# Performance work log

Hardware: AMD Instinct MI355X
Metric: run time of the kernel (lower is better)

Reference implementation:

```python
import jax, jax.numpy as jnp
import numpy as np

D_MODEL, NHEAD, D_K = 512, 8, 64
MIN_RBF, MAX_RBF = 0.1, 0.9
MIN_SPREAD, MAX_SPREAD, BASE = 1.0, 6.0, 20.0
LN_EPS = 1e-5


def _layernorm(x, w, b):
    mu = jnp.mean(x, axis=-1, keepdims=True)
    var = jnp.var(x, axis=-1, keepdims=True)
    return (x - mu) * jax.lax.rsqrt(var + LN_EPS) * w + b


def setup_inputs() -> dict:
    key = jax.random.key(0)
    ks = jax.random.split(key, 10)
    B, N = 1, 2048
    inp = {
        "q": jax.random.normal(ks[0], (B, N, D_MODEL), jnp.float32),
        "k": jax.random.normal(ks[1], (B, N, D_MODEL), jnp.float32),
        "v": jax.random.normal(ks[2], (B, N, D_MODEL), jnp.float32),
        "coords": jax.random.normal(ks[3], (B, N, 3), jnp.float32) * 3.0,
        "key_padding_mask": jnp.zeros((B, N), bool),
        # learned params (torch.randn init for projections, LN defaults)
        "q_proj": jax.random.normal(ks[4], (NHEAD, D_MODEL, D_K), jnp.float32),
        "k_proj": jax.random.normal(ks[5], (NHEAD, D_MODEL, D_K), jnp.float32),
        "v_proj": jax.random.normal(ks[6], (NHEAD, D_MODEL, D_K), jnp.float32),
        "q_ln_w": jnp.ones((D_K,), jnp.float32), "q_ln_b": jnp.zeros((D_K,), jnp.float32),
        "k_ln_w": jnp.ones((D_K,), jnp.float32), "k_ln_b": jnp.zeros((D_K,), jnp.float32),
        "v_ln_w": jnp.ones((D_K,), jnp.float32), "v_ln_b": jnp.zeros((D_K,), jnp.float32),
        "out_w": jax.random.normal(ks[7], (D_MODEL, D_MODEL), jnp.float32) / np.sqrt(D_MODEL),
        "out_b": jnp.zeros((D_MODEL,), jnp.float32),
    }
    return inp


def reference(q, k, v, coords, key_padding_mask,
              q_proj, k_proj, v_proj,
              q_ln_w, q_ln_b, k_ln_w, k_ln_b, v_ln_w, v_ln_b,
              out_w, out_b):
    B, N, _ = q.shape
    # per-head projections: [B,H,N,dk]
    Q = _layernorm(jnp.einsum('bnd,hdk->bhnk', q, q_proj), q_ln_w, q_ln_b)
    K = _layernorm(jnp.einsum('bnd,hdk->bhnk', k, k_proj), k_ln_w, k_ln_b)
    V = _layernorm(jnp.einsum('bnd,hdk->bhnk', v, v_proj), v_ln_w, v_ln_b)

    # head-specific gaussian spreads (torch.logspace(0,1,H,base) semantics)
    spreads = MIN_SPREAD + (MAX_SPREAD - MIN_SPREAD) * (BASE ** jnp.linspace(0.0, 1.0, NHEAD) - 1.0) / (BASE - 1.0)

    # pairwise squared distances [B,N,N] -> per-head RBF [B,H,N,N]
    d2 = jnp.sum((coords[:, :, None, :] - coords[:, None, :, :]) ** 2, axis=-1)
    rbf = jnp.exp(-d2[:, None, :, :] / (2.0 * spreads[None, :, None, None] ** 2))
    rbf = jnp.clip(rbf, MIN_RBF, MAX_RBF)

    # RBF-modulated scaled dot-product attention
    scores = jnp.einsum('bhik,bhjk->bhij', Q, K) / np.sqrt(D_K) * rbf
    scores = jnp.where(key_padding_mask[:, None, None, :], -1e9, scores)
    P = jax.nn.softmax(scores, axis=-1)
    out = jnp.einsum('bhij,bhjk->bhik', P, V)  # [B,H,N,dk]

    # torch: out.permute(0,2,3,1).reshape(B,N,d_model)
    out = jnp.transpose(out, (0, 2, 3, 1)).reshape(B, N, D_MODEL)
    return out @ out_w.T + out_b
```

## Files before the change

### kernel.cpp

```cpp
#include <hip/hip_runtime.h>
#include <math.h>

#define N_TOK 2048
#define D_MODEL 512
#define NHEAD 8
#define DK 64
#define LOG2E 1.44269504f
#define QSCALE 0.18033688f
#define KTILE 6144
#define KHEAD (32 * KTILE)

typedef __attribute__((ext_vector_type(8))) short short8;
typedef __attribute__((ext_vector_type(4))) short short4v;
typedef __attribute__((ext_vector_type(4))) float f32x4;
typedef __attribute__((ext_vector_type(16))) float f32x16;
typedef __attribute__((ext_vector_type(4))) unsigned int u32x4;

__device__ __forceinline__ short f2bf(float x) {
    unsigned u = __float_as_uint(x);
    u = (u + 0x7fffu + ((u >> 16) & 1u)) >> 16;
    return (short)u;
}

__device__ __forceinline__ float bf2f(short s) {
    return __uint_as_float(((unsigned)(unsigned short)s) << 16);
}

__device__ __forceinline__ void split2(float x, short& h_, short& l_) {
    h_ = f2bf(x);
    l_ = f2bf(x - bf2f(h_));
}

__device__ __forceinline__ void split3(float x, short& h_, short& m_, short& l_) {
    h_ = f2bf(x);
    float r = x - bf2f(h_);
    m_ = f2bf(r);
    l_ = f2bf(r - bf2f(m_));
}

__device__ __forceinline__ unsigned cvt_pk_bf16(float lo, float hi) {
    unsigned r;
    asm("v_cvt_pk_bf16_f32 %0, %1, %2" : "=v"(r) : "v"(lo), "v"(hi));
    return r;
}

__device__ __forceinline__ float head_c(int h) {
    float tt = (float)h * (1.0f / 7.0f);
    float sp = 1.0f + 5.0f * (__builtin_exp2f(tt * 4.3219281f) - 1.0f) * (1.0f / 19.0f);
    return -LOG2E / (2.0f * sp * sp);
}

__global__ __launch_bounds__(256) void prep_all_kernel(
    const float* __restrict__ coords, const unsigned char* __restrict__ mask,
    const float* __restrict__ qp, const float* __restrict__ kp,
    const float* __restrict__ vp, const float* __restrict__ ow,
    short* __restrict__ Wt, short* __restrict__ Wo,
    short* __restrict__ Kf, float* __restrict__ mpen,
    unsigned* __restrict__ tflag)
{
    __shared__ float tile[64][65];
    const int bid = blockIdx.x;
    const int t = threadIdx.x;

    if (bid < 256) {
        int i = bid;
        int z = i >> 6;
        int bx = i & 7, by = (i >> 3) & 7;
        if (z == 3) {
            int m0 = bx * 64, j0 = by * 64, hh = by;
            for (int ii = t; ii < 4096; ii += 256) {
                int r = ii >> 6, kk = ii & 63;
                Wo[(size_t)(m0 + r) * 512 + j0 + kk] =
                    f2bf(ow[(size_t)(m0 + r) * 512 + kk * 8 + hh]);
            }
            return;
        }
        const float* src = z == 0 ? qp : (z == 1 ? kp : vp);
        const int h = bx, d0 = by * 64;
        for (int ii = t; ii < 4096; ii += 256) {
            int r = ii >> 6, c = ii & 63;
            tile[r][c] = src[((size_t)h * 512 + d0 + r) * 64 + c];
        }
        __syncthreads();
        short* W = Wt + (size_t)z * 512 * 512;
        for (int ii = t; ii < 4096; ii += 256) {
            int cr = ii >> 6, dc_ = ii & 63;
            W[(size_t)(h * 64 + cr) * 512 + d0 + dc_] = f2bf(tile[dc_][cr]);
        }
    } else {
        int j = (bid - 256) * 256 + t;
        float x = coords[j * 3 + 0], y = coords[j * 3 + 1], z = coords[j * 3 + 2];
        unsigned char mk = mask[j];
        mpen[j] = mk ? -1e9f : 0.f;
        unsigned long long b = __ballot(mk != 0);
        if ((t & 63) == 0) tflag[j >> 6] = (b != 0ull) ? 1u : 0u;
        float n2 = x * x + y * y + z * z;
        const short one = (short)0x3F80;
        const int s = (j & 63) >> 5;
        const int m = j & 31;
        #pragma unroll
        for (int h = 0; h < NHEAD; ++h) {
            float c = head_c(h);
            short ahx, alx, ahy, aly, ahz, alz, k2a, k2b, k2c;
            split2(-2.f * c * x, ahx, alx);
            split2(-2.f * c * y, ahy, aly);
            split2(-2.f * c * z, ahz, alz);
            split3(c * n2, k2a, k2b, k2c);
            short8 g0, g1, g2, g3;
            g0[0] = ahx; g0[1] = alx; g0[2] = ahx; g0[3] = ahy;
            g0[4] = aly; g0[5] = ahy; g0[6] = ahz; g0[7] = alz;
            g1[0] = ahz; g1[1] = alx; g1[2] = aly; g1[3] = alz;
            g1[4] = k2a; g1[5] = k2b; g1[6] = k2c; g1[7] = one;
            g2[0] = one; g2[1] = one;
            #pragma unroll
            for (int e = 2; e < 8; ++e) g2[e] = 0;
            #pragma unroll
            for (int e = 0; e < 8; ++e) g3[e] = 0;
            short* base = Kf + (size_t)h * KHEAD + (size_t)(j >> 6) * KTILE
                        + 4096 + (size_t)s * 1024;
            *(short8*)(base + (size_t)m * 8) = g0;
            *(short8*)(base + (size_t)(m + 32) * 8) = g1;
            *(short8*)(base + 512 + (size_t)m * 8) = g2;
            *(short8*)(base + 512 + (size_t)(m + 32) * 8) = g3;
        }
    }
}

__global__ __launch_bounds__(256) void proj_ln_mfma_kernel(
    const float* __restrict__ xq, const float* __restrict__ xk,
    const float* __restrict__ xv, const short* __restrict__ Wt,
    const float* __restrict__ qlw, const float* __restrict__ qlb,
    const float* __restrict__ klw, const float* __restrict__ klb,
    const float* __restrict__ vlw, const float* __restrict__ vlb,
    short* __restrict__ Qf, short* __restrict__ Kf, short* __restrict__ Vf)
{
    __shared__ short Xs[128 * 64];
    __shared__ short Ws[64 * 64];
    const int z = blockIdx.z, h = blockIdx.y;
    const int n0 = blockIdx.x * 128;
    const int tid = threadIdx.x, w = tid >> 6, l = tid & 63;
    const int l15 = l & 15, lg = l >> 4;

    const float* X = z == 0 ? xq : (z == 1 ? xk : xv);
    const short* Wz = Wt + ((size_t)z * 512 + h * 64) * 512;

    const f32x4 zero4 = {0.f, 0.f, 0.f, 0.f};
    f32x4 acc[2][4];
    #pragma unroll
    for (int H = 0; H < 2; ++H)
        #pragma unroll
        for (int dc = 0; dc < 4; ++dc) acc[H][dc] = zero4;

    for (int kb = 0; kb < 8; ++kb) {
        const int d0 = kb * 64;
        __syncthreads();
        #pragma unroll
        for (int i = 0; i < 8; ++i) {
            int idx = tid + i * 256;
            int r = idx >> 4;
            int f = idx & 15;
            float4 xv4 = *(const float4*)(X + (size_t)(n0 + r) * 512 + d0 + f * 4);
            short4v pk;
            pk[0] = f2bf(xv4.x); pk[1] = f2bf(xv4.y);
            pk[2] = f2bf(xv4.z); pk[3] = f2bf(xv4.w);
            *(short4v*)(Xs + r * 64 + (((f >> 1) * 8) ^ ((r & 7) << 3)) + (f & 1) * 4) = pk;
        }
        #pragma unroll
        for (int i = 0; i < 2; ++i) {
            int c = tid + i * 256;
            int r = c >> 3, g = c & 7;
            short8 wv = *(const short8*)(Wz + (size_t)r * 512 + d0 + g * 8);
            *(short8*)(Ws + r * 64 + ((g * 8) ^ ((r & 7) << 3))) = wv;
        }
        __syncthreads();
        const int arowA = w * 16 + l15;
        const int arowB = 64 + arowA;
        const int asw = (arowA & 7) << 3;
        short8 aA0 = *(const short8*)(Xs + arowA * 64 + ((lg * 8) ^ asw));
        short8 aA1 = *(const short8*)(Xs + arowA * 64 + ((32 + lg * 8) ^ asw));
        short8 aB0 = *(const short8*)(Xs + arowB * 64 + ((lg * 8) ^ asw));
        short8 aB1 = *(const short8*)(Xs + arowB * 64 + ((32 + lg * 8) ^ asw));
        #pragma unroll
        for (int dc = 0; dc < 4; ++dc) {
            const int brow = dc * 16 + l15;
            short8 b0 = *(const short8*)(Ws + brow * 64 + ((lg * 8) ^ ((brow & 7) << 3)));
            short8 b1 = *(const short8*)(Ws + brow * 64 + ((32 + lg * 8) ^ ((brow & 7) << 3)));
            acc[0][dc] = __builtin_amdgcn_mfma_f32_16x16x32_bf16(aA0, b0, acc[0][dc], 0, 0, 0);
            acc[0][dc] = __builtin_amdgcn_mfma_f32_16x16x32_bf16(aA1, b1, acc[0][dc], 0, 0, 0);
            acc[1][dc] = __builtin_amdgcn_mfma_f32_16x16x32_bf16(aB0, b0, acc[1][dc], 0, 0, 0);
            acc[1][dc] = __builtin_amdgcn_mfma_f32_16x16x32_bf16(aB1, b1, acc[1][dc], 0, 0, 0);
        }
    }

    const float* lw  = z == 0 ? qlw : (z == 1 ? klw : vlw);
    const float* lbp = z == 0 ? qlb : (z == 1 ? klb : vlb);
    float wv_[4], bv_[4];
    #pragma unroll
    for (int dc = 0; dc < 4; ++dc) {
        wv_[dc] = lw[dc * 16 + l15];
        bv_[dc] = lbp[dc * 16 + l15];
    }

    #pragma unroll
    for (int H = 0; H < 2; ++H) {
        const int nb = n0 + H * 64;
        const int kt = nb >> 6;
        float mu[4], rs[4];
        #pragma unroll
        for (int reg = 0; reg < 4; ++reg) {
            float s = acc[H][0][reg] + acc[H][1][reg] + acc[H][2][reg] + acc[H][3][reg];
            #pragma unroll
            for (int off = 1; off < 16; off <<= 1) s += __shfl_xor(s, off);
            float m = s * (1.0f / 64.0f);
            float ss = 0.f;
            #pragma unroll
            for (int dc = 0; dc < 4; ++dc) { float d = acc[H][dc][reg] - m; ss += d * d; }
            #pragma unroll
            for (int off = 1; off < 16; off <<= 1) ss += __shfl_xor(ss, off);
            mu[reg] = m;
            rs[reg] = rsqrtf(ss * (1.0f / 64.0f) + 1e-5f);
        }
        if (z == 0) {
            short* Qh = Qf + (size_t)h * (N_TOK * DK);
            #pragma unroll
            for (int dc = 0; dc < 4; ++dc)
                #pragma unroll
                for (int reg = 0; reg < 4; ++reg) {
                    int n = nb + w * 16 + lg * 4 + reg;
                    float val = ((acc[H][dc][reg] - mu[reg]) * rs[reg] * wv_[dc] + bv_[dc]) * QSCALE;
                    size_t addr = (size_t)(n >> 5) * 2048 + dc * 512
                                + ((n & 31) + 32 * (l15 >> 3)) * 8 + (l15 & 7);
                    Qh[addr] = f2bf(val);
                }
        } else if (z == 1) {
            short* Kh = Kf + (size_t)h * KHEAD;
            const int sA = w >> 1;
            const int mA = (w & 1) * 16 + lg * 4;
            #pragma unroll
            for (int dc = 0; dc < 4; ++dc)
                #pragma unroll
                for (int reg = 0; reg < 4; ++reg) {
                    float val = (acc[H][dc][reg] - mu[reg]) * rs[reg] * wv_[dc] + bv_[dc];
                    size_t addr = (size_t)kt * KTILE + sA * 2048 + dc * 512
                                + (mA + reg + 32 * (l15 >> 3)) * 8 + (l15 & 7);
                    Kh[addr] = f2bf(val);
                }
        } else {
            short* Vh = Vf + (size_t)h * (N_TOK * DK);
            const int kc = w;
            const int g = lg >> 1;
            const int e0 = (lg & 1) * 4;
            #pragma unroll
            for (int dc = 0; dc < 4; ++dc) {
                int dt = dc >> 1;
                int m = (dc & 1) * 16 + l15;
                short4v p;
                #pragma unroll
                for (int reg = 0; reg < 4; ++reg)
                    p[reg] = f2bf((acc[H][dc][reg] - mu[reg]) * rs[reg] * wv_[dc] + bv_[dc]);
                size_t addr = (size_t)kt * 4096 + dt * 2048 + kc * 512
                            + (m + 32 * g) * 8 + e0;
                *(short4v*)(Vh + addr) = p;
            }
        }
    }
}

__global__ __launch_bounds__(256) void attn_kernel(
    const short* __restrict__ Qf, const short* __restrict__ Kf,
    const short* __restrict__ Vf, const float* __restrict__ coords,
    const float* __restrict__ mpen, const unsigned* __restrict__ tflag,
    short* __restrict__ PO, float* __restrict__ PL)
{
    __shared__ float bufO[2][32][65];
    __shared__ float bufL[2][32];

    const int tid = threadIdx.x;
    const int w = tid >> 6, l = tid & 63;
    const int q31 = l & 31;
    const bool hi = (l >= 32);
    const int rbase = hi ? 4 : 0;
    const int bid = blockIdx.x;
    const int h  = bid & 7;
    const int qt = (bid >> 3) & 63;
    const int z  = bid >> 9;
    const int n0 = qt * 32;

    const short* qbase = Qf + (size_t)h * (N_TOK * DK) + (size_t)qt * 2048 + l * 8;
    short8 qf[4];
    #pragma unroll
    for (int c = 0; c < 4; ++c) qf[c] = *(const short8*)(qbase + c * 512);

    const float ch = head_c(h);
    const int qn = n0 + q31;
    const float qx = coords[qn * 3 + 0];
    const float qy = coords[qn * 3 + 1];
    const float qz = coords[qn * 3 + 2];
    const float cq2 = ch * (qx * qx + qy * qy + qz * qz);
    short8 qaug0, qaug1;
    {
        const short one = (short)0x3F80;
        short qhx, qlx, qhy, qly, qhz, qlz, q2a, q2b, q2c;
        split2(qx, qhx, qlx);
        split2(qy, qhy, qly);
        split2(qz, qhz, qlz);
        split3(cq2, q2a, q2b, q2c);
        if (!hi) {
            qaug0[0] = qhx; qaug0[1] = qhx; qaug0[2] = qlx; qaug0[3] = qhy;
            qaug0[4] = qhy; qaug0[5] = qly; qaug0[6] = qhz; qaug0[7] = qhz;
            qaug1[0] = q2b; qaug1[1] = q2c;
            #pragma unroll
            for (int e = 2; e < 8; ++e) qaug1[e] = 0;
        } else {
            qaug0[0] = qlz; qaug0[1] = qlx; qaug0[2] = qly; qaug0[3] = qlz;
            qaug0[4] = one; qaug0[5] = one; qaug0[6] = one; qaug0[7] = q2a;
            #pragma unroll
            for (int e = 0; e < 8; ++e) qaug1[e] = 0;
        }
    }

    const f32x16 zero16 = {0,0,0,0, 0,0,0,0, 0,0,0,0, 0,0,0,0};
    f32x16 oacc0 = zero16, oacc1 = zero16;
    float l_ = 0.f;

    const short* Kfh = Kf + (size_t)h * KHEAD;
    const short* Vfh = Vf + (size_t)h * (N_TOK * DK);

    for (int t = 0; t < 4; ++t) {
        const int kt = z * 16 + w * 4 + t;
        const int kbase = kt * 64;
        #pragma unroll
        for (int s = 0; s < 2; ++s) {
            const short* kp = Kfh + (size_t)kt * KTILE + s * 2048 + l * 8;
            const short* ap = Kfh + (size_t)kt * KTILE + 4096 + s * 1024 + l * 8;
            const short* vp = Vfh + (size_t)kt * 4096 + s * 1024 + l * 8;

            f32x16 sacc = zero16, aacc = zero16;
            #pragma unroll
            for (int c = 0; c < 4; ++c) {
                short8 kfr = *(const short8*)(kp + c * 512);
                sacc = __builtin_amdgcn_mfma_f32_32x32x16_bf16(kfr, qf[c], sacc, 0, 0, 0);
            }
            {
                short8 a0 = *(const short8*)(ap);
                short8 a1 = *(const short8*)(ap + 512);
                aacc = __builtin_amdgcn_mfma_f32_32x32x16_bf16(a0, qaug0, aacc, 0, 0, 0);
                aacc = __builtin_amdgcn_mfma_f32_32x32x16_bf16(a1, qaug1, aacc, 0, 0, 0);
            }

            #pragma unroll
            for (int r = 0; r < 16; ++r) {
                float rb = __builtin_exp2f(aacc[r]);
                rb = fminf(fmaxf(rb, 0.1f), 0.9f);
                sacc[r] *= rb;
            }
            if (tflag[kt]) {
                #pragma unroll
                for (int r = 0; r < 16; ++r)
                    sacc[r] += mpen[kbase + s * 32 + ((r & 3) + 8 * (r >> 2) + rbase)];
            }

            #pragma unroll
            for (int r = 0; r < 16; ++r) sacc[r] = __builtin_exp2f(sacc[r]);
            {
                float s01 = (sacc[0] + sacc[1]) + (sacc[2] + sacc[3]);
                float s23 = (sacc[4] + sacc[5]) + (sacc[6] + sacc[7]);
                float s45 = (sacc[8] + sacc[9]) + (sacc[10] + sacc[11]);
                float s67 = (sacc[12] + sacc[13]) + (sacc[14] + sacc[15]);
                l_ += (s01 + s23) + (s45 + s67);
            }

            unsigned U0 = cvt_pk_bf16(sacc[0], sacc[1]);
            unsigned U1 = cvt_pk_bf16(sacc[2], sacc[3]);
            unsigned U2 = cvt_pk_bf16(sacc[4], sacc[5]);
            unsigned U3 = cvt_pk_bf16(sacc[6], sacc[7]);
            unsigned U4 = cvt_pk_bf16(sacc[8], sacc[9]);
            unsigned U5 = cvt_pk_bf16(sacc[10], sacc[11]);
            unsigned U6 = cvt_pk_bf16(sacc[12], sacc[13]);
            unsigned U7 = cvt_pk_bf16(sacc[14], sacc[15]);
            unsigned W0 = (unsigned)__shfl_xor((int)U0, 32);
            unsigned W1 = (unsigned)__shfl_xor((int)U1, 32);
            unsigned W2 = (unsigned)__shfl_xor((int)U2, 32);
            unsigned W3 = (unsigned)__shfl_xor((int)U3, 32);
            unsigned W4 = (unsigned)__shfl_xor((int)U4, 32);
            unsigned W5 = (unsigned)__shfl_xor((int)U5, 32);
            unsigned W6 = (unsigned)__shfl_xor((int)U6, 32);
            unsigned W7 = (unsigned)__shfl_xor((int)U7, 32);

            u32x4 b0v, b1v;
            b0v[0] = hi ? W2 : U0;  b0v[1] = hi ? W3 : U1;
            b0v[2] = hi ? U2 : W0;  b0v[3] = hi ? U3 : W1;
            b1v[0] = hi ? W6 : U4;  b1v[1] = hi ? W7 : U5;
            b1v[2] = hi ? U6 : W4;  b1v[3] = hi ? U7 : W5;
            short8 pb0 = __builtin_bit_cast(short8, b0v);
            short8 pb1 = __builtin_bit_cast(short8, b1v);

            {
                short8 v00 = *(const short8*)(vp);
                short8 v01 = *(const short8*)(vp + 512);
                short8 v10 = *(const short8*)(vp + 2048);
                short8 v11 = *(const short8*)(vp + 2048 + 512);
                oacc0 = __builtin_amdgcn_mfma_f32_32x32x16_bf16(v00, pb0, oacc0, 0, 0, 0);
                oacc0 = __builtin_amdgcn_mfma_f32_32x32x16_bf16(v01, pb1, oacc0, 0, 0, 0);
                oacc1 = __builtin_amdgcn_mfma_f32_32x32x16_bf16(v10, pb0, oacc1, 0, 0, 0);
                oacc1 = __builtin_amdgcn_mfma_f32_32x32x16_bf16(v11, pb1, oacc1, 0, 0, 0);
            }
        }
    }

    l_ += __shfl_xor(l_, 32);

    if (w >= 2) {
        int slot = w - 2;
        if (!hi) bufL[slot][q31] = l_;
        #pragma unroll
        for (int r = 0; r < 16; ++r) {
            int d = (r & 3) + 8 * (r >> 2) + rbase;
            bufO[slot][q31][d] = oacc0[r];
            bufO[slot][q31][32 + d] = oacc1[r];
        }
    }
    __syncthreads();
    if (w < 2) {
        l_ += bufL[w][q31];
        #pragma unroll
        for (int r = 0; r < 16; ++r) {
            int d = (r & 3) + 8 * (r >> 2) + rbase;
            oacc0[r] += bufO[w][q31][d];
            oacc1[r] += bufO[w][q31][32 + d];
        }
    }
    __syncthreads();
    if (w == 1) {
        if (!hi) bufL[0][q31] = l_;
        #pragma unroll
        for (int r = 0; r < 16; ++r) {
            int d = (r & 3) + 8 * (r >> 2) + rbase;
            bufO[0][q31][d] = oacc0[r];
            bufO[0][q31][32 + d] = oacc1[r];
        }
    }
    __syncthreads();
    if (w == 0) {
        l_ += bufL[0][q31];
        size_t p = ((size_t)z * NHEAD + h) * N_TOK + n0 + q31;
        if (!hi) PL[p] = l_;
        #pragma unroll
        for (int r = 0; r < 16; ++r) {
            int d = (r & 3) + 8 * (r >> 2) + rbase;
            PO[p * 64 + d] = f2bf(oacc0[r] + bufO[0][q31][d]);
            PO[p * 64 + 32 + d] = f2bf(oacc1[r] + bufO[0][q31][32 + d]);
        }
    }
}

__global__ __launch_bounds__(256) void out_proj_kernel(
    const short* __restrict__ PO, const float* __restrict__ PL,
    const short* __restrict__ Wo, const float* __restrict__ bias,
    float* __restrict__ out)
{
    __shared__ short As[64 * 64];
    __shared__ short Bs[64 * 64];
    const int n0 = blockIdx.x * 64, m0 = blockIdx.y * 64;
    const int tid = threadIdx.x, w = tid >> 6, l = tid & 63;
    const int l15 = l & 15, lg = l >> 4;

    const f32x4 zero4 = {0.f, 0.f, 0.f, 0.f};
    f32x4 acc[4];
    #pragma unroll
    for (int dc = 0; dc < 4; ++dc) acc[dc] = zero4;

    for (int kb = 0; kb < 8; ++kb) {
        const int j0 = kb * 64;
        __syncthreads();
        #pragma unroll
        for (int i = 0; i < 2; ++i) {
            int c = tid + i * 256;
            int r = c >> 3, g = c & 7;
            int n = n0 + r;
            size_t p0 = (size_t)kb * N_TOK + n;
            size_t p1 = (size_t)(NHEAD + kb) * N_TOK + n;
            float rl = 1.0f / (PL[p0] + PL[p1]);
            short8 a0 = *(const short8*)(PO + p0 * 64 + g * 8);
            short8 a1 = *(const short8*)(PO + p1 * 64 + g * 8);
            short8 av;
            #pragma unroll
            for (int e = 0; e < 8; ++e)
                av[e] = f2bf((bf2f(a0[e]) + bf2f(a1[e])) * rl);
            *(short8*)(As + r * 64 + ((g * 8) ^ ((r & 7) << 3))) = av;
            short8 bv = *(const short8*)(Wo + (size_t)(m0 + r) * 512 + j0 + g * 8);
            *(short8*)(Bs + r * 64 + ((g * 8) ^ ((r & 7) << 3))) = bv;
        }
        __syncthreads();
        const int arow = w * 16 + l15;
        short8 a0 = *(const short8*)(As + arow * 64 + ((lg * 8) ^ ((arow & 7) << 3)));
        short8 a1 = *(const short8*)(As + arow * 64 + ((32 + lg * 8) ^ ((arow & 7) << 3)));
        #pragma unroll
        for (int dc = 0; dc < 4; ++dc) {
            const int brow = dc * 16 + l15;
            short8 b0 = *(const short8*)(Bs + brow * 64 + ((lg * 8) ^ ((brow & 7) << 3)));
            acc[dc] = __builtin_amdgcn_mfma_f32_16x16x32_bf16(a0, b0, acc[dc], 0, 0, 0);
            short8 b1 = *(const short8*)(Bs + brow * 64 + ((32 + lg * 8) ^ ((brow & 7) << 3)));
            acc[dc] = __builtin_amdgcn_mfma_f32_16x16x32_bf16(a1, b1, acc[dc], 0, 0, 0);
        }
    }

    #pragma unroll
    for (int dc = 0; dc < 4; ++dc) {
        float bm = bias[m0 + dc * 16 + l15];
        #pragma unroll
        for (int reg = 0; reg < 4; ++reg) {
            int n = n0 + w * 16 + lg * 4 + reg;
            out[(size_t)n * D_MODEL + m0 + dc * 16 + l15] = acc[dc][reg] + bm;
        }
    }
}

extern "C" void kernel_launch(void* const* d_in, const int* in_sizes, int n_in,
                              void* d_out, int out_size, void* d_ws, size_t ws_size,
                              hipStream_t stream)
{
    const float* q      = (const float*)d_in[0];
    const float* k      = (const float*)d_in[1];
    const float* v      = (const float*)d_in[2];
    const float* coords = (const float*)d_in[3];
    const unsigned char* mask = (const unsigned char*)d_in[4];
    const float* q_proj = (const float*)d_in[5];
    const float* k_proj = (const float*)d_in[6];
    const float* v_proj = (const float*)d_in[7];
    const float* q_ln_w = (const float*)d_in[8];
    const float* q_ln_b = (const float*)d_in[9];
    const float* k_ln_w = (const float*)d_in[10];
    const float* k_ln_b = (const float*)d_in[11];
    const float* v_ln_w = (const float*)d_in[12];
    const float* v_ln_b = (const float*)d_in[13];
    const float* out_w  = (const float*)d_in[14];
    const float* out_b  = (const float*)d_in[15];
    float* out = (float*)d_out;

    short* PO  = (short*)d_ws;
    short* Wt  = PO + 2097152;
    short* Wo  = Wt + 786432;
    short* Qf  = Wo + 262144;
    short* Kf  = Qf + 1048576;
    short* Vf  = Kf + 1572864;
    float* mpen = (float*)(Vf + 1048576);
    unsigned* tflag = (unsigned*)(mpen + 2048);
    float* PL = (float*)(tflag + 32);

    prep_all_kernel<<<dim3(264), dim3(256), 0, stream>>>(
        coords, mask, q_proj, k_proj, v_proj, out_w, Wt, Wo, Kf, mpen, tflag);
    proj_ln_mfma_kernel<<<dim3(16, 8, 3), dim3(256), 0, stream>>>(
        q, k, v, Wt, q_ln_w, q_ln_b, k_ln_w, k_ln_b, v_ln_w, v_ln_b, Qf, Kf, Vf);
    attn_kernel<<<dim3(1024), dim3(256), 0, stream>>>(
        Qf, Kf, Vf, coords, mpen, tflag, PO, PL);
    out_proj_kernel<<<dim3(32, 8), dim3(256), 0, stream>>>(PO, PL, Wo, out_b, out);
}
```

Before: 67.18 us.

## Write per-wave attention partials to global and reduce them in out-proj

Removes the in-block LDS tree reduction of the four waves' partial O and L (three __syncthreads and the shared buffers) in the attention kernel. Each wave now writes its own bf16 partial output and row sum to global memory as one of eight key-split parts, and the out-projection kernel sums all eight parts while loading its A tile. This trades barrier and LDS traffic for four times more partial-output global writes and reads, a larger workspace, and extra bf16 rounding of partials before summation.

```diff
diff --git a/kernel.cpp b/kernel.cpp
--- a/kernel.cpp
+++ b/kernel.cpp
@@ -9,6 +9,7 @@
 #define QSCALE 0.18033688f
 #define KTILE 6144
 #define KHEAD (32 * KTILE)
+#define KSPLIT 8
 
 typedef __attribute__((ext_vector_type(8))) short short8;
 typedef __attribute__((ext_vector_type(4))) short short4v;
@@ -272,9 +273,6 @@
     const float* __restrict__ mpen, const unsigned* __restrict__ tflag,
     short* __restrict__ PO, float* __restrict__ PL)
 {
-    __shared__ float bufO[2][32][65];
-    __shared__ float bufL[2][32];
-
     const int tid = threadIdx.x;
     const int w = tid >> 6, l = tid & 63;
     const int q31 = l & 31;
@@ -285,6 +283,7 @@
     const int qt = (bid >> 3) & 63;
     const int z  = bid >> 9;
     const int n0 = qt * 32;
+    const int part = z * 4 + w;
 
     const short* qbase = Qf + (size_t)h * (N_TOK * DK) + (size_t)qt * 2048 + l * 8;
     short8 qf[4];
@@ -410,47 +409,18 @@
 
     l_ += __shfl_xor(l_, 32);
 
-    if (w >= 2) {
-        int slot = w - 2;
-        if (!hi) bufL[slot][q31] = l_;
-        #pragma unroll
-        for (int r = 0; r < 16; ++r) {
-            int d = (r & 3) + 8 * (r >> 2) + rbase;
-            bufO[slot][q31][d] = oacc0[r];
-            bufO[slot][q31][32 + d] = oacc1[r];
-        }
-    }
-    __syncthreads();
-    if (w < 2) {
-        l_ += bufL[w][q31];
-        #pragma unroll
-        for (int r = 0; r < 16; ++r) {
-            int d = (r & 3) + 8 * (r >> 2) + rbase;
-            oacc0[r] += bufO[w][q31][d];
-            oacc1[r] += bufO[w][q31][32 + d];
-        }
-    }
-    __syncthreads();
-    if (w == 1) {
-        if (!hi) bufL[0][q31] = l_;
-        #pragma unroll
-        for (int r = 0; r < 16; ++r) {
-            int d = (r & 3) + 8 * (r >> 2) + rbase;
-            bufO[0][q31][d] = oacc0[r];
-            bufO[0][q31][32 + d] = oacc1[r];
-        }
-    }
-    __syncthreads();
-    if (w == 0) {
-        l_ += bufL[0][q31];
-        size_t p = ((size_t)z * NHEAD + h) * N_TOK + n0 + q31;
-        if (!hi) PL[p] = l_;
-        #pragma unroll
-        for (int r = 0; r < 16; ++r) {
-            int d = (r & 3) + 8 * (r >> 2) + rbase;
-            PO[p * 64 + d] = f2bf(oacc0[r] + bufO[0][q31][d]);
-            PO[p * 64 + 32 + d] = f2bf(oacc1[r] + bufO[0][q31][32 + d]);
-        }
+    size_t p = ((size_t)part * NHEAD + h) * N_TOK + n0 + q31;
+    if (!hi) PL[p] = l_;
+    #pragma unroll
+    for (int g2 = 0; g2 < 4; ++g2) {
+        short4v o0, o1;
+        #pragma unroll
+        for (int e = 0; e < 4; ++e) {
+            o0[e] = f2bf(oacc0[g2 * 4 + e]);
+            o1[e] = f2bf(oacc1[g2 * 4 + e]);
+        }
+        *(short4v*)(PO + p * 64 + 8 * g2 + rbase) = o0;
+        *(short4v*)(PO + p * 64 + 32 + 8 * g2 + rbase) = o1;
     }
 }
 
@@ -478,15 +448,22 @@
             int c = tid + i * 256;
             int r = c >> 3, g = c & 7;
             int n = n0 + r;
-            size_t p0 = (size_t)kb * N_TOK + n;
-            size_t p1 = (size_t)(NHEAD + kb) * N_TOK + n;
-            float rl = 1.0f / (PL[p0] + PL[p1]);
-            short8 a0 = *(const short8*)(PO + p0 * 64 + g * 8);
-            short8 a1 = *(const short8*)(PO + p1 * 64 + g * 8);
+            float le = 0.f;
+            float se[8];
+            #pragma unroll
+            for (int e = 0; e < 8; ++e) se[e] = 0.f;
+            #pragma unroll
+            for (int pp = 0; pp < KSPLIT; ++pp) {
+                size_t pbase = ((size_t)pp * NHEAD + kb) * N_TOK + n;
+                le += PL[pbase];
+                short8 ax = *(const short8*)(PO + pbase * 64 + g * 8);
+                #pragma unroll
+                for (int e = 0; e < 8; ++e) se[e] += bf2f(ax[e]);
+            }
+            float rl = 1.0f / le;
             short8 av;
             #pragma unroll
-            for (int e = 0; e < 8; ++e)
-                av[e] = f2bf((bf2f(a0[e]) + bf2f(a1[e])) * rl);
+            for (int e = 0; e < 8; ++e) av[e] = f2bf(se[e] * rl);
             *(short8*)(As + r * 64 + ((g * 8) ^ ((r & 7) << 3))) = av;
             short8 bv = *(const short8*)(Wo + (size_t)(m0 + r) * 512 + j0 + g * 8);
             *(short8*)(Bs + r * 64 + ((g * 8) ^ ((r & 7) << 3))) = bv;
@@ -539,7 +516,7 @@
     float* out = (float*)d_out;
 
     short* PO  = (short*)d_ws;
-    short* Wt  = PO + 2097152;
+    short* Wt  = PO + 8388608;
     short* Wo  = Wt + 786432;
     short* Qf  = Wo + 262144;
     short* Kf  = Qf + 1048576;
```

Measured after the change: 108.9 us. 62.1% more time.
